# Performance work log

Hardware: AMD Instinct MI355X
Metric: run time of the kernel (lower is better)

Reference implementation:

```python
import jax, jax.numpy as jnp
import numpy as np

B, S, D, H = 4, 2048, 1024, 16
DH = D // H


def setup_inputs() -> dict:
    key = jax.random.key(0)
    ks = jax.random.split(key, 10)
    scale = 1.0 / np.sqrt(D)
    return {
        "query": jax.random.normal(ks[0], (B, S, D), dtype=jnp.float32),
        "mask": jax.random.randint(ks[1], (B, S, S), 0, 2).astype(jnp.bool_),
        "Wq": jax.random.normal(ks[2], (D, D), dtype=jnp.float32) * scale,
        "bq": jax.random.normal(ks[3], (D,), dtype=jnp.float32) * 0.01,
        "Wk": jax.random.normal(ks[4], (D, D), dtype=jnp.float32) * scale,
        "bk": jax.random.normal(ks[5], (D,), dtype=jnp.float32) * 0.01,
        "Wv": jax.random.normal(ks[6], (D, D), dtype=jnp.float32) * scale,
        "bv": jax.random.normal(ks[7], (D,), dtype=jnp.float32) * 0.01,
        "Wo": jax.random.normal(ks[8], (D, D), dtype=jnp.float32) * scale,
        "bo": jax.random.normal(ks[9], (D,), dtype=jnp.float32) * 0.01,
    }


def reference(query, mask, Wq, bq, Wk, bk, Wv, bv, Wo, bo):
    # Self-attention path (key=value=None): q,k,v all from `query`.
    # Linear layers use torch convention: x @ W.T + b.  [B,S,D]
    q = query @ Wq.T + bq
    k = query @ Wk.T + bk
    v = query @ Wv.T + bv

    # split heads: [B,S,D] -> [B,H,S,DH]
    def split(x):
        return x.reshape(B, S, H, DH).transpose(0, 2, 1, 3)

    q, k, v = split(q), split(k), split(v)

    # scaled dot-product scores: [B,H,Sq,Sk]
    scores = jnp.einsum("bhqd,bhkd->bhqk", q, k) / jnp.sqrt(
        jnp.asarray(DH, dtype=q.dtype)
    )
    # MULTIPLICATIVE mask (True where masked), broadcast over heads
    scores = scores * mask[:, None, :, :].astype(scores.dtype)

    attn = jax.nn.softmax(scores, axis=-1)  # [B,H,Sq,Sk]
    out = jnp.einsum("bhqk,bhkd->bhqd", attn, v)  # [B,H,Sq,DH]

    # merge heads: [B,H,S,DH] -> [B,S,D]
    out = out.transpose(0, 2, 1, 3).reshape(B, S, D)
    return out @ Wo.T + bo
```

## Files before the change

### kernel.cpp

```cpp
#include <hip/hip_runtime.h>
#include <hip/hip_bf16.h>

#define DEVINL __device__ __forceinline__

typedef __attribute__((ext_vector_type(8))) short bf16x8;
typedef __attribute__((ext_vector_type(4))) float f32x4;

static constexpr int Bb = 4, Ss = 2048, Dd = 1024, Hh = 16, DHh = 64;
#define QPRESCALE 0.18033688f
#define DEFER_THR 11.5f

DEVINL unsigned short f2bf(float f) {
  union { float f; unsigned int u; } a; a.f = f;
  unsigned int u = a.u;
  return (unsigned short)((u + 0x7fffu + ((u >> 16) & 1u)) >> 16);
}

DEVINL float fexp2(float x) {
#if __has_builtin(__builtin_amdgcn_exp2f)
  return __builtin_amdgcn_exp2f(x);
#else
  return __builtin_exp2f(x);
#endif
}

DEVINL void gload16(const void* g, void* l) {
  __builtin_amdgcn_global_load_lds((const __attribute__((address_space(1))) void*)g,
                                   (__attribute__((address_space(3))) void*)l, 16, 0, 0);
}

__global__ void cvt_f32_bf16(const float4* __restrict__ src, ushort* __restrict__ dst, int n4) {
  int i = blockIdx.x * blockDim.x + threadIdx.x;
  int stride = gridDim.x * blockDim.x;
  for (; i < n4; i += stride) {
    float4 v = src[i];
    ushort4 o;
    o.x = f2bf(v.x); o.y = f2bf(v.y); o.z = f2bf(v.z); o.w = f2bf(v.w);
    *reinterpret_cast<ushort4*>(dst + (size_t)i * 4) = o;
  }
}

__global__ void bias_cat(const float* __restrict__ bq, const float* __restrict__ bk,
                         const float* __restrict__ bv, float* __restrict__ bcat) {
  int i = blockIdx.x * blockDim.x + threadIdx.x;
  if (i < 1024) bcat[i] = bq[i];
  else if (i < 2048) bcat[i] = bk[i - 1024];
  else if (i < 3072) bcat[i] = bv[i - 2048];
}

__global__ void mask_bits(const int* __restrict__ mask, unsigned long long* __restrict__ bm) {
  const int tid = threadIdx.x, lane = tid & 63;
  const int gw = blockIdx.x * 4 + (tid >> 6);
  const int b = gw >> 16;
  const int rem = gw & 65535;
  const int s = rem >> 5, ch = rem & 31;
  int m = mask[((size_t)b * Ss + s) * Ss + ch * 64 + lane];
  unsigned long long bits = __ballot(m != 0);
  if (lane == 0) bm[((size_t)b * 32 + ch) * Ss + s] = bits;
}

template<int OUT_BF16, int QSCALE>
__global__ __launch_bounds__(256)
void gemm_bt(const ushort* __restrict__ A, const ushort* __restrict__ Bm,
             const float* __restrict__ bias, void* __restrict__ Cout,
             int M, int N, int K) {
  __shared__ short lA[128 * 32];
  __shared__ short lB[128 * 32];
  const int tid = threadIdx.x;
  const int lane = tid & 63;
  const int wid = tid >> 6;
  const int wm = wid >> 1, wn = wid & 1;
  const int row0 = blockIdx.x * 128, col0 = blockIdx.y * 128;
  const int lr = lane & 15, lk8 = (lane >> 4) * 8;

  f32x4 acc[4][4];
#pragma unroll
  for (int i = 0; i < 4; i++)
#pragma unroll
    for (int j = 0; j < 4; j++) acc[i][j] = (f32x4){0.f, 0.f, 0.f, 0.f};

  const int c0 = tid, c1 = tid + 256;
  const int r0s = c0 >> 2, k0s = c0 & 3;
  const int r1s = c1 >> 2, k1s = c1 & 3;

  for (int kk = 0; kk < K; kk += 32) {
    __syncthreads();
    gload16(A + (size_t)(row0 + r0s) * K + kk + k0s * 8, lA + c0 * 8);
    gload16(A + (size_t)(row0 + r1s) * K + kk + k1s * 8, lA + c1 * 8);
    gload16(Bm + (size_t)(col0 + r0s) * K + kk + k0s * 8, lB + c0 * 8);
    gload16(Bm + (size_t)(col0 + r1s) * K + kk + k1s * 8, lB + c1 * 8);
    __syncthreads();

    bf16x8 af[4], bfr[4];
#pragma unroll
    for (int i = 0; i < 4; i++)
      af[i] = *reinterpret_cast<const bf16x8*>(&lA[(wm * 64 + i * 16 + lr) * 32 + lk8]);
#pragma unroll
    for (int j = 0; j < 4; j++)
      bfr[j] = *reinterpret_cast<const bf16x8*>(&lB[(wn * 64 + j * 16 + lr) * 32 + lk8]);
#pragma unroll
    for (int i = 0; i < 4; i++)
#pragma unroll
      for (int j = 0; j < 4; j++)
        acc[i][j] = __builtin_amdgcn_mfma_f32_16x16x32_bf16(af[i], bfr[j], acc[i][j], 0, 0, 0);
  }

#pragma unroll
  for (int j = 0; j < 4; j++) {
    const int c = col0 + wn * 64 + j * 16 + lr;
    const float bv = bias[c];
    const float qs = (QSCALE && c < 1024) ? QPRESCALE : 1.0f;
#pragma unroll
    for (int i = 0; i < 4; i++) {
      const int rbase = row0 + wm * 64 + i * 16 + (lane >> 4) * 4;
#pragma unroll
      for (int t = 0; t < 4; t++) {
        float v = (acc[i][j][t] + bv) * qs;
        if (OUT_BF16)
          reinterpret_cast<ushort*>(Cout)[(size_t)(rbase + t) * N + c] = f2bf(v);
        else
          reinterpret_cast<float*>(Cout)[(size_t)(rbase + t) * N + c] = v;
      }
    }
  }
}

__global__ __launch_bounds__(256)
void attn_fwd(const ushort* __restrict__ qkv, const unsigned long long* __restrict__ bmask,
              ushort* __restrict__ ctx) {
  const int qt = blockIdx.x, h = blockIdx.y, b = blockIdx.z;
  const int tid = threadIdx.x, lane = tid & 63, wid = tid >> 6;
  const int q0 = qt * 64;
  const int lr = lane & 15, lg = lane >> 4;
  const int RS = 3072;

  __shared__ short lK[64 * 64];
  __shared__ short lV[64 * 64];
  __shared__ short lP[4][16 * 64];
  __shared__ unsigned long long lM[64];

  const size_t rowb = (size_t)b * Ss;

  bf16x8 qf[2];
  {
    const ushort* gq = qkv + (rowb + q0 + wid * 16 + lr) * RS + h * 64;
    qf[0] = *reinterpret_cast<const bf16x8*>(gq + lg * 8);
    qf[1] = *reinterpret_cast<const bf16x8*>(gq + 32 + lg * 8);
  }

  f32x4 oacc[4];
#pragma unroll
  for (int j = 0; j < 4; j++) oacc[j] = (f32x4){0.f, 0.f, 0.f, 0.f};
  float mrun[4], lp[4];
#pragma unroll
  for (int r = 0; r < 4; r++) { mrun[r] = -1e30f; lp[r] = 0.f; }

  const int sr = tid >> 2, sseg = tid & 3;

  for (int t = 0; t < Ss / 64; ++t) {
    __syncthreads();
    {
      const ushort* Kg = qkv + (rowb + t * 64) * RS + 1024 + h * 64;
      int c = tid, row = c >> 3, c7 = c & 7;
      gload16(Kg + (size_t)row * RS + ((c7 ^ (row & 7)) * 8), ((char*)lK) + c * 16);
      c = tid + 256; row = c >> 3; c7 = c & 7;
      gload16(Kg + (size_t)row * RS + ((c7 ^ (row & 7)) * 8), ((char*)lK) + c * 16);
    }
    {
      const ushort* gv = qkv + (rowb + t * 64 + sr) * RS + 2048 + h * 64 + sseg * 16;
      bf16x8 y0 = *reinterpret_cast<const bf16x8*>(gv);
      bf16x8 y1 = *reinterpret_cast<const bf16x8*>(gv + 8);
#pragma unroll
      for (int j2 = 0; j2 < 8; j2++) {
        int d = sseg * 16 + j2;
        lV[d * 64 + (sr ^ ((j2 ^ sseg) << 3))] = y0[j2];
      }
#pragma unroll
      for (int j2 = 0; j2 < 8; j2++) {
        int d = sseg * 16 + 8 + j2;
        lV[d * 64 + (sr ^ ((j2 ^ sseg) << 3))] = y1[j2];
      }
    }
    if (tid < 64) lM[tid] = bmask[((size_t)b * 32 + t) * Ss + q0 + tid];
    __syncthreads();

    f32x4 sc[4];
    __builtin_amdgcn_s_setprio(1);
#pragma unroll
    for (int f = 0; f < 4; ++f) {
      const int row = f * 16 + lr;
      const int s0 = (lg ^ (lr & 7)) * 8;
      bf16x8 kb0 = *reinterpret_cast<const bf16x8*>(&lK[row * 64 + s0]);
      bf16x8 kb1 = *reinterpret_cast<const bf16x8*>(&lK[row * 64 + (s0 ^ 32)]);
      f32x4 z = (f32x4){0.f, 0.f, 0.f, 0.f};
      z = __builtin_amdgcn_mfma_f32_16x16x32_bf16(qf[0], kb0, z, 0, 0, 0);
      z = __builtin_amdgcn_mfma_f32_16x16x32_bf16(qf[1], kb1, z, 0, 0, 0);
      sc[f] = z;
    }
    __builtin_amdgcn_s_setprio(0);

    float pv[4][4];
    float tmax = -1e30f;
#pragma unroll
    for (int r = 0; r < 4; ++r) {
      const unsigned long long m64 = lM[wid * 16 + lg * 4 + r];
      const unsigned wlo = (unsigned)m64, whi = (unsigned)(m64 >> 32);
#pragma unroll
      for (int f = 0; f < 4; ++f) {
        const unsigned w = (f & 2) ? whi : wlo;
        const int sh = ((f & 1) << 4) + lr;
        float sv = ((w >> sh) & 1u) ? sc[f][r] : 0.0f;
        pv[f][r] = sv;
        tmax = fmaxf(tmax, sv);
      }
    }
#pragma unroll
    for (int off = 1; off < 64; off <<= 1) tmax = fmaxf(tmax, __shfl_xor(tmax, off, 64));
    const float minm = fminf(fminf(mrun[0], mrun[1]), fminf(mrun[2], mrun[3]));
    if (!__all(tmax <= minm + DEFER_THR)) {
#pragma unroll
      for (int r = 0; r < 4; ++r) {
        float rm = fmaxf(fmaxf(pv[0][r], pv[1][r]), fmaxf(pv[2][r], pv[3][r]));
#pragma unroll
        for (int off = 1; off < 16; off <<= 1) rm = fmaxf(rm, __shfl_xor(rm, off, 64));
        const float mn = fmaxf(mrun[r], rm);
        const float al = fexp2(mrun[r] - mn);
        mrun[r] = mn;
        lp[r] *= al;
#pragma unroll
        for (int j = 0; j < 4; j++) oacc[j][r] *= al;
      }
    }
#pragma unroll
    for (int r = 0; r < 4; ++r)
#pragma unroll
      for (int f = 0; f < 4; ++f) {
        float p = fexp2(pv[f][r] - mrun[r]);
        pv[f][r] = p;
        lp[r] += p;
      }

    short* pw = &lP[wid][0];
#pragma unroll
    for (int r = 0; r < 4; r++) {
      const int q = lg * 4 + r;
      const int swp = (q >> 2) << 4;
#pragma unroll
      for (int f = 0; f < 4; f++)
        pw[q * 64 + ((f * 16 + lr) ^ swp)] = (short)f2bf(pv[f][r]);
    }
    __builtin_amdgcn_wave_barrier();
    {
      const int swp = (lr >> 2) << 4;
      bf16x8 pa0 = *reinterpret_cast<const bf16x8*>(&pw[lr * 64 + ((lg * 8) ^ swp)]);
      bf16x8 pa1 = *reinterpret_cast<const bf16x8*>(&pw[lr * 64 + ((32 + lg * 8) ^ swp)]);
      __builtin_amdgcn_s_setprio(1);
#pragma unroll
      for (int j = 0; j < 4; ++j) {
        const int d = j * 16 + lr;
        const int sv2 = ((lr & 7) ^ j) << 3;
        bf16x8 vb0 = *reinterpret_cast<const bf16x8*>(&lV[d * 64 + ((lg * 8) ^ sv2)]);
        bf16x8 vb1 = *reinterpret_cast<const bf16x8*>(&lV[d * 64 + ((32 + lg * 8) ^ sv2)]);
        oacc[j] = __builtin_amdgcn_mfma_f32_16x16x32_bf16(pa0, vb0, oacc[j], 0, 0, 0);
        oacc[j] = __builtin_amdgcn_mfma_f32_16x16x32_bf16(pa1, vb1, oacc[j], 0, 0, 0);
      }
      __builtin_amdgcn_s_setprio(0);
    }
    __builtin_amdgcn_wave_barrier();
  }

#pragma unroll
  for (int r = 0; r < 4; ++r) {
#pragma unroll
    for (int off = 1; off < 16; off <<= 1) lp[r] += __shfl_xor(lp[r], off, 64);
  }
  float invl[4];
#pragma unroll
  for (int r = 0; r < 4; r++) invl[r] = 1.0f / lp[r];
#pragma unroll
  for (int j = 0; j < 4; j++)
#pragma unroll
    for (int r = 0; r < 4; r++) {
      const int row = q0 + wid * 16 + lg * 4 + r;
      const int col = h * DHh + j * 16 + lr;
      ctx[(rowb + row) * Dd + col] = (short)f2bf(oacc[j][r] * invl[r]);
    }
}

extern "C" void kernel_launch(void* const* d_in, const int* in_sizes, int n_in,
                              void* d_out, int out_size, void* d_ws, size_t ws_size,
                              hipStream_t stream) {
  const float* query = (const float*)d_in[0];
  const int* mask = (const int*)d_in[1];
  const float* Wq = (const float*)d_in[2];
  const float* bq = (const float*)d_in[3];
  const float* Wk = (const float*)d_in[4];
  const float* bk = (const float*)d_in[5];
  const float* Wv = (const float*)d_in[6];
  const float* bv = (const float*)d_in[7];
  const float* Wo = (const float*)d_in[8];
  const float* bo = (const float*)d_in[9];
  float* out = (float*)d_out;

  ushort* ws = (ushort*)d_ws;
  const size_t SZ_X = (size_t)8192 * 1024;
  ushort* xB   = ws;
  ushort* ctx  = ws;
  ushort* qkvB = ws + SZ_X;
  ushort* wcat = qkvB + (size_t)8192 * 3072;
  ushort* woB  = wcat + (size_t)3072 * 1024;
  float*  bcat = (float*)(woB + (size_t)1024 * 1024);
  unsigned long long* bmask = (unsigned long long*)((char*)bcat + 16384);

  dim3 blk(256);
  cvt_f32_bf16<<<2048, blk, 0, stream>>>((const float4*)query, xB, (int)(SZ_X / 4));
  cvt_f32_bf16<<<512, blk, 0, stream>>>((const float4*)Wq, wcat, 1024 * 1024 / 4);
  cvt_f32_bf16<<<512, blk, 0, stream>>>((const float4*)Wk, wcat + 1048576, 1024 * 1024 / 4);
  cvt_f32_bf16<<<512, blk, 0, stream>>>((const float4*)Wv, wcat + 2097152, 1024 * 1024 / 4);
  cvt_f32_bf16<<<512, blk, 0, stream>>>((const float4*)Wo, woB, 1024 * 1024 / 4);
  bias_cat<<<12, blk, 0, stream>>>(bq, bk, bv, bcat);
  mask_bits<<<65536, blk, 0, stream>>>(mask, bmask);

  dim3 gqkv(64, 24);
  gemm_bt<1, 1><<<gqkv, blk, 0, stream>>>(xB, wcat, bcat, qkvB, 8192, 3072, 1024);

  dim3 ga(32, 16, 4);
  attn_fwd<<<ga, blk, 0, stream>>>(qkvB, bmask, ctx);

  dim3 go(64, 8);
  gemm_bt<0, 0><<<go, blk, 0, stream>>>(ctx, woB, bo, out, 8192, 1024, 1024);
}
```

Baseline: 453.2 us.

## Write V transposed from QKV GEMM and load V tile via async LDS copies

The QKV GEMM epilogue now writes the V projection transposed into a separate buffer, so the attention kernel can fill its V tile with direct global-to-LDS loads instead of per-element scattered LDS stores. The mask bits are read straight from global into registers rather than staged through shared memory. The lazy-rescale test becomes per-row rather than a wave-wide max reduction, and the trailing wave barrier is dropped. The transposed V store uses strided 8-byte writes, which could be less coalesced in the GEMM epilogue.

```diff
diff --git a/kernel.cpp b/kernel.cpp
--- a/kernel.cpp
+++ b/kernel.cpp
@@ -16,13 +16,12 @@
   return (unsigned short)((u + 0x7fffu + ((u >> 16) & 1u)) >> 16);
 }
 
-DEVINL float fexp2(float x) {
-#if __has_builtin(__builtin_amdgcn_exp2f)
-  return __builtin_amdgcn_exp2f(x);
-#else
-  return __builtin_exp2f(x);
-#endif
-}
+DEVINL unsigned short f2bf_rne(float f) {
+  __hip_bfloat16 h = __float2bfloat16(f);
+  return *reinterpret_cast<unsigned short*>(&h);
+}
+
+DEVINL float fexp2(float x) { return __builtin_exp2f(x); }
 
 DEVINL void gload16(const void* g, void* l) {
   __builtin_amdgcn_global_load_lds((const __attribute__((address_space(1))) void*)g,
@@ -63,7 +62,7 @@
 __global__ __launch_bounds__(256)
 void gemm_bt(const ushort* __restrict__ A, const ushort* __restrict__ Bm,
              const float* __restrict__ bias, void* __restrict__ Cout,
-             int M, int N, int K) {
+             ushort* __restrict__ vT, int M, int N, int K, int ldc) {
   __shared__ short lA[128 * 32];
   __shared__ short lB[128 * 32];
   const int tid = threadIdx.x;
@@ -105,41 +104,66 @@
         acc[i][j] = __builtin_amdgcn_mfma_f32_16x16x32_bf16(af[i], bfr[j], acc[i][j], 0, 0, 0);
   }
 
-#pragma unroll
-  for (int j = 0; j < 4; j++) {
-    const int c = col0 + wn * 64 + j * 16 + lr;
-    const float bv = bias[c];
-    const float qs = (QSCALE && c < 1024) ? QPRESCALE : 1.0f;
-#pragma unroll
-    for (int i = 0; i < 4; i++) {
-      const int rbase = row0 + wm * 64 + i * 16 + (lane >> 4) * 4;
-#pragma unroll
-      for (int t = 0; t < 4; t++) {
-        float v = (acc[i][j][t] + bv) * qs;
-        if (OUT_BF16)
-          reinterpret_cast<ushort*>(Cout)[(size_t)(rbase + t) * N + c] = f2bf(v);
-        else
-          reinterpret_cast<float*>(Cout)[(size_t)(rbase + t) * N + c] = v;
+  if (QSCALE && col0 >= 2048) {
+#pragma unroll
+    for (int j = 0; j < 4; j++) {
+      const int c = col0 + wn * 64 + j * 16 + lr;
+      const float bv = bias[c];
+      const int d = c - 2048;
+#pragma unroll
+      for (int i = 0; i < 4; i++) {
+        const int rbase = row0 + wm * 64 + i * 16 + (lane >> 4) * 4;
+        ushort4 o;
+        o.x = f2bf_rne(acc[i][j][0] + bv);
+        o.y = f2bf_rne(acc[i][j][1] + bv);
+        o.z = f2bf_rne(acc[i][j][2] + bv);
+        o.w = f2bf_rne(acc[i][j][3] + bv);
+        *reinterpret_cast<ushort4*>(&vT[(size_t)d * 8192 + rbase]) = o;
+      }
+    }
+  } else {
+#pragma unroll
+    for (int j = 0; j < 4; j++) {
+      const int c = col0 + wn * 64 + j * 16 + lr;
+      const float bv = bias[c];
+      const float qs = (QSCALE && c < 1024) ? QPRESCALE : 1.0f;
+#pragma unroll
+      for (int i = 0; i < 4; i++) {
+        const int rbase = row0 + wm * 64 + i * 16 + (lane >> 4) * 4;
+#pragma unroll
+        for (int t = 0; t < 4; t++) {
+          float v = (acc[i][j][t] + bv) * qs;
+          if (OUT_BF16)
+            reinterpret_cast<ushort*>(Cout)[(size_t)(rbase + t) * ldc + c] = f2bf_rne(v);
+          else
+            reinterpret_cast<float*>(Cout)[(size_t)(rbase + t) * ldc + c] = v;
+        }
       }
     }
   }
 }
 
 __global__ __launch_bounds__(256)
-void attn_fwd(const ushort* __restrict__ qkv, const unsigned long long* __restrict__ bmask,
-              ushort* __restrict__ ctx) {
+void attn_fwd(const ushort* __restrict__ qkv, const ushort* __restrict__ vT,
+              const unsigned long long* __restrict__ bmask, ushort* __restrict__ ctx) {
   const int qt = blockIdx.x, h = blockIdx.y, b = blockIdx.z;
   const int tid = threadIdx.x, lane = tid & 63, wid = tid >> 6;
   const int q0 = qt * 64;
   const int lr = lane & 15, lg = lane >> 4;
-  const int RS = 3072;
+  const int RS = 2048;
 
   __shared__ short lK[64 * 64];
-  __shared__ short lV[64 * 64];
+  __shared__ short lVt[64 * 64];
   __shared__ short lP[4][16 * 64];
-  __shared__ unsigned long long lM[64];
 
   const size_t rowb = (size_t)b * Ss;
+  const ushort* Kg = qkv + rowb * RS + 1024 + h * 64;
+  const ushort* Vtg = vT + (size_t)(h * 64) * 8192 + b * 2048;
+  const unsigned long long* Mg = bmask + (size_t)b * 32 * Ss + q0 + wid * 16 + lg * 4;
+
+  const int kn0 = tid, kn1 = tid + 256;
+  const int k_r0 = kn0 >> 3, k_c0 = ((kn0 & 7) ^ (k_r0 & 7)) * 8;
+  const int k_r1 = kn1 >> 3, k_c1 = ((kn1 & 7) ^ (k_r1 & 7)) * 8;
 
   bf16x8 qf[2];
   {
@@ -155,41 +179,26 @@
 #pragma unroll
   for (int r = 0; r < 4; r++) { mrun[r] = -1e30f; lp[r] = 0.f; }
 
-  const int sr = tid >> 2, sseg = tid & 3;
-
   for (int t = 0; t < Ss / 64; ++t) {
     __syncthreads();
+    gload16(Kg + ((size_t)t * 64 + k_r0) * RS + k_c0, lK + kn0 * 8);
+    gload16(Kg + ((size_t)t * 64 + k_r1) * RS + k_c1, lK + kn1 * 8);
+    gload16(Vtg + (size_t)k_r0 * 8192 + t * 64 + k_c0, lVt + kn0 * 8);
+    gload16(Vtg + (size_t)k_r1 * 8192 + t * 64 + k_c1, lVt + kn1 * 8);
+    ulonglong2 mq0, mq1;
     {
-      const ushort* Kg = qkv + (rowb + t * 64) * RS + 1024 + h * 64;
-      int c = tid, row = c >> 3, c7 = c & 7;
-      gload16(Kg + (size_t)row * RS + ((c7 ^ (row & 7)) * 8), ((char*)lK) + c * 16);
-      c = tid + 256; row = c >> 3; c7 = c & 7;
-      gload16(Kg + (size_t)row * RS + ((c7 ^ (row & 7)) * 8), ((char*)lK) + c * 16);
-    }
-    {
-      const ushort* gv = qkv + (rowb + t * 64 + sr) * RS + 2048 + h * 64 + sseg * 16;
-      bf16x8 y0 = *reinterpret_cast<const bf16x8*>(gv);
-      bf16x8 y1 = *reinterpret_cast<const bf16x8*>(gv + 8);
-#pragma unroll
-      for (int j2 = 0; j2 < 8; j2++) {
-        int d = sseg * 16 + j2;
-        lV[d * 64 + (sr ^ ((j2 ^ sseg) << 3))] = y0[j2];
-      }
-#pragma unroll
-      for (int j2 = 0; j2 < 8; j2++) {
-        int d = sseg * 16 + 8 + j2;
-        lV[d * 64 + (sr ^ ((j2 ^ sseg) << 3))] = y1[j2];
-      }
-    }
-    if (tid < 64) lM[tid] = bmask[((size_t)b * 32 + t) * Ss + q0 + tid];
+      const ulonglong2* mp_ = (const ulonglong2*)(Mg + (size_t)t * Ss);
+      mq0 = mp_[0];
+      mq1 = mp_[1];
+    }
     __syncthreads();
 
     f32x4 sc[4];
+    const int s0 = (lg ^ (lr & 7)) * 8;
     __builtin_amdgcn_s_setprio(1);
 #pragma unroll
     for (int f = 0; f < 4; ++f) {
       const int row = f * 16 + lr;
-      const int s0 = (lg ^ (lr & 7)) * 8;
       bf16x8 kb0 = *reinterpret_cast<const bf16x8*>(&lK[row * 64 + s0]);
       bf16x8 kb1 = *reinterpret_cast<const bf16x8*>(&lK[row * 64 + (s0 ^ 32)]);
       f32x4 z = (f32x4){0.f, 0.f, 0.f, 0.f};
@@ -199,28 +208,27 @@
     }
     __builtin_amdgcn_s_setprio(0);
 
-    float pv[4][4];
-    float tmax = -1e30f;
-#pragma unroll
-    for (int r = 0; r < 4; ++r) {
-      const unsigned long long m64 = lM[wid * 16 + lg * 4 + r];
-      const unsigned wlo = (unsigned)m64, whi = (unsigned)(m64 >> 32);
-#pragma unroll
-      for (int f = 0; f < 4; ++f) {
-        const unsigned w = (f & 2) ? whi : wlo;
-        const int sh = ((f & 1) << 4) + lr;
-        float sv = ((w >> sh) & 1u) ? sc[f][r] : 0.0f;
-        pv[f][r] = sv;
-        tmax = fmaxf(tmax, sv);
-      }
-    }
-#pragma unroll
-    for (int off = 1; off < 64; off <<= 1) tmax = fmaxf(tmax, __shfl_xor(tmax, off, 64));
-    const float minm = fminf(fminf(mrun[0], mrun[1]), fminf(mrun[2], mrun[3]));
-    if (!__all(tmax <= minm + DEFER_THR)) {
+    float pvv[4][4], lmax[4];
+    {
+      const unsigned long long mm_[4] = {mq0.x, mq0.y, mq1.x, mq1.y};
 #pragma unroll
       for (int r = 0; r < 4; ++r) {
-        float rm = fmaxf(fmaxf(pv[0][r], pv[1][r]), fmaxf(pv[2][r], pv[3][r]));
+        const unsigned wlo = (unsigned)mm_[r], whi = (unsigned)(mm_[r] >> 32);
+#pragma unroll
+        for (int f = 0; f < 4; ++f) {
+          const unsigned w = (f & 2) ? whi : wlo;
+          const int sh = ((f & 1) << 4) + lr;
+          pvv[f][r] = ((w >> sh) & 1u) ? sc[f][r] : 0.0f;
+        }
+        lmax[r] = fmaxf(fmaxf(pvv[0][r], pvv[1][r]), fmaxf(pvv[2][r], pvv[3][r]));
+      }
+    }
+    bool ok_ = (lmax[0] <= mrun[0] + DEFER_THR) & (lmax[1] <= mrun[1] + DEFER_THR) &
+               (lmax[2] <= mrun[2] + DEFER_THR) & (lmax[3] <= mrun[3] + DEFER_THR);
+    if (!__all(ok_)) {
+#pragma unroll
+      for (int r = 0; r < 4; ++r) {
+        float rm = lmax[r];
 #pragma unroll
         for (int off = 1; off < 16; off <<= 1) rm = fmaxf(rm, __shfl_xor(rm, off, 64));
         const float mn = fmaxf(mrun[r], rm);
@@ -235,8 +243,8 @@
     for (int r = 0; r < 4; ++r)
 #pragma unroll
       for (int f = 0; f < 4; ++f) {
-        float p = fexp2(pv[f][r] - mrun[r]);
-        pv[f][r] = p;
+        float p = fexp2(pvv[f][r] - mrun[r]);
+        pvv[f][r] = p;
         lp[r] += p;
       }
 
@@ -247,26 +255,24 @@
       const int swp = (q >> 2) << 4;
 #pragma unroll
       for (int f = 0; f < 4; f++)
-        pw[q * 64 + ((f * 16 + lr) ^ swp)] = (short)f2bf(pv[f][r]);
+        pw[q * 64 + ((f * 16 + lr) ^ swp)] = (short)f2bf_rne(pvv[f][r]);
     }
     __builtin_amdgcn_wave_barrier();
     {
-      const int swp = (lr >> 2) << 4;
-      bf16x8 pa0 = *reinterpret_cast<const bf16x8*>(&pw[lr * 64 + ((lg * 8) ^ swp)]);
-      bf16x8 pa1 = *reinterpret_cast<const bf16x8*>(&pw[lr * 64 + ((32 + lg * 8) ^ swp)]);
+      const int swp2 = (lr >> 2) << 4;
+      bf16x8 pa0 = *reinterpret_cast<const bf16x8*>(&pw[lr * 64 + ((lg * 8) ^ swp2)]);
+      bf16x8 pa1 = *reinterpret_cast<const bf16x8*>(&pw[lr * 64 + ((32 + lg * 8) ^ swp2)]);
       __builtin_amdgcn_s_setprio(1);
 #pragma unroll
       for (int j = 0; j < 4; ++j) {
-        const int d = j * 16 + lr;
-        const int sv2 = ((lr & 7) ^ j) << 3;
-        bf16x8 vb0 = *reinterpret_cast<const bf16x8*>(&lV[d * 64 + ((lg * 8) ^ sv2)]);
-        bf16x8 vb1 = *reinterpret_cast<const bf16x8*>(&lV[d * 64 + ((32 + lg * 8) ^ sv2)]);
+        const int row = j * 16 + lr;
+        bf16x8 vb0 = *reinterpret_cast<const bf16x8*>(&lVt[row * 64 + s0]);
+        bf16x8 vb1 = *reinterpret_cast<const bf16x8*>(&lVt[row * 64 + (s0 ^ 32)]);
         oacc[j] = __builtin_amdgcn_mfma_f32_16x16x32_bf16(pa0, vb0, oacc[j], 0, 0, 0);
         oacc[j] = __builtin_amdgcn_mfma_f32_16x16x32_bf16(pa1, vb1, oacc[j], 0, 0, 0);
       }
       __builtin_amdgcn_s_setprio(0);
     }
-    __builtin_amdgcn_wave_barrier();
   }
 
 #pragma unroll
@@ -283,7 +289,7 @@
     for (int r = 0; r < 4; r++) {
       const int row = q0 + wid * 16 + lg * 4 + r;
       const int col = h * DHh + j * 16 + lr;
-      ctx[(rowb + row) * Dd + col] = (short)f2bf(oacc[j][r] * invl[r]);
+      ctx[(rowb + row) * Dd + col] = (short)f2bf_rne(oacc[j][r] * invl[r]);
     }
 }
 
@@ -307,10 +313,11 @@
   ushort* xB   = ws;
   ushort* ctx  = ws;
   ushort* qkvB = ws + SZ_X;
-  ushort* wcat = qkvB + (size_t)8192 * 3072;
+  ushort* wcat = qkvB + (size_t)8192 * 2048;
   ushort* woB  = wcat + (size_t)3072 * 1024;
   float*  bcat = (float*)(woB + (size_t)1024 * 1024);
   unsigned long long* bmask = (unsigned long long*)((char*)bcat + 16384);
+  ushort* vT   = (ushort*)((char*)bmask + (size_t)2 * 1024 * 1024);
 
   dim3 blk(256);
   cvt_f32_bf16<<<2048, blk, 0, stream>>>((const float4*)query, xB, (int)(SZ_X / 4));
@@ -322,11 +329,11 @@
   mask_bits<<<65536, blk, 0, stream>>>(mask, bmask);
 
   dim3 gqkv(64, 24);
-  gemm_bt<1, 1><<<gqkv, blk, 0, stream>>>(xB, wcat, bcat, qkvB, 8192, 3072, 1024);
+  gemm_bt<1, 1><<<gqkv, blk, 0, stream>>>(xB, wcat, bcat, qkvB, vT, 8192, 3072, 1024, 2048);
 
   dim3 ga(32, 16, 4);
-  attn_fwd<<<ga, blk, 0, stream>>>(qkvB, bmask, ctx);
+  attn_fwd<<<ga, blk, 0, stream>>>(qkvB, vT, bmask, ctx);
 
   dim3 go(64, 8);
-  gemm_bt<0, 0><<<go, blk, 0, stream>>>(ctx, woB, bo, out, 8192, 1024, 1024);
-}
+  gemm_bt<0, 0><<<go, blk, 0, stream>>>(ctx, woB, bo, out, nullptr, 8192, 1024, 1024, 1024);
+}
```

After: 460.7 us. No clear change (+1.6%).
